# Kernel optimization log

Hardware: AMD Instinct MI355X
Metric: run time of the kernel (lower is better)

## Reference

```python
import jax, jax.numpy as jnp
import numpy as np

T0, T1, LENGTH = 844, 1264, 8137


def setup_inputs() -> dict:
    key = jax.random.key(0)
    kq, = jax.random.split(key, 1)
    q = jax.random.normal(kq, (4, 8, LENGTH), dtype=jnp.float32)
    alpha0 = jnp.array(0.4886, dtype=jnp.float32)
    alpha1 = jnp.array(0.3893, dtype=jnp.float32)
    return {"q": q, "alpha0": alpha0, "alpha1": alpha1}


def reference(q, alpha0, alpha1):
    # A = I + alpha0 * superdiag(offset T0) + alpha1 * superdiag(offset T1)
    A = (jnp.eye(LENGTH, dtype=q.dtype)
         + alpha0 * jnp.eye(LENGTH, k=T0, dtype=q.dtype)
         + alpha1 * jnp.eye(LENGTH, k=T1, dtype=q.dtype))
    A_inv = jnp.linalg.inv(A)          # [L, L] dense inverse
    x = q @ A_inv                       # [B, C, L]
    loss = jnp.sum(x[0, 0, -T1:] ** 2)  # scalar
    return loss
```

## Files before the change

### kernel.cpp

```cpp
#include <hip/hip_runtime.h>


#define LENGTH 8137
#define T0 844
#define T1 1264
#define JSTART (LENGTH - T1)
#define MMAX 9
#define NMAX 6

__global__ __launch_bounds__(256) void iir_loss_kernel(const float* __restrict__ q,
                                                       const float* __restrict__ a0p,
                                                       const float* __restrict__ a1p,
                                                       float* __restrict__ out) {
    __shared__ float xq[LENGTH];
    __shared__ float coef[NMAX + 1][MMAX + 1];
    __shared__ float partial[4];

    const int tid = threadIdx.x;
    const float a0 = a0p[0];
    const float a1 = a1p[0];

    const float4* q4 = reinterpret_cast<const float4*>(q);
    for (int i = tid; i < LENGTH / 4; i += 256) {
        float4 v = q4[i];
        xq[4 * i + 0] = v.x;
        xq[4 * i + 1] = v.y;
        xq[4 * i + 2] = v.z;
        xq[4 * i + 3] = v.w;
    }
    if (tid == 0) {
        xq[LENGTH - 1] = q[LENGTH - 1];
        coef[0][0] = 1.f;
        for (int m = 1; m <= MMAX; ++m) coef[0][m] = -a0 * coef[0][m - 1];
        for (int n = 1; n <= NMAX; ++n) {
            coef[n][0] = -a1 * coef[n - 1][0];
            for (int m = 1; m <= MMAX; ++m)
                coef[n][m] = -a0 * coef[n][m - 1] - a1 * coef[n - 1][m];
        }
    }
    __syncthreads();

    float v0 = 0.f, v1 = 0.f, v2 = 0.f, v3 = 0.f, v4 = 0.f;
    const int j0 = JSTART + tid;
    const bool has4 = (tid < (T1 - 4 * 256));

    for (int n = 0; n <= NMAX; ++n) {
        const int sn = T1 * n;
        for (int m = 0; m <= MMAX; ++m) {
            const int shift = sn + T0 * m;
            if (shift >= LENGTH) break;
            const float c = coef[n][m];
            const int off = j0 - shift;
            if (off >= 0)                 v0 += c * xq[off];
            if (off + 256 >= 0)           v1 += c * xq[off + 256];
            if (off + 512 >= 0)           v2 += c * xq[off + 512];
            if (off + 768 >= 0)           v3 += c * xq[off + 768];
            if (has4 && off + 1024 >= 0)  v4 += c * xq[off + 1024];
        }
    }

    float s = v0 * v0 + v1 * v1 + v2 * v2 + v3 * v3 + v4 * v4;

    for (int off = 32; off > 0; off >>= 1)
        s += __shfl_down(s, off, 64);
    if ((tid & 63) == 0) partial[tid >> 6] = s;
    __syncthreads();
    if (tid == 0)
        out[0] = partial[0] + partial[1] + partial[2] + partial[3];
}

extern "C" void kernel_launch(void* const* d_in, const int* in_sizes, int n_in,
                              void* d_out, int out_size, void* d_ws, size_t ws_size,
                              hipStream_t stream) {
    const float* q      = (const float*)d_in[0];
    const float* alpha0 = (const float*)d_in[1];
    const float* alpha1 = (const float*)d_in[2];
    float* out = (float*)d_out;

    iir_loss_kernel<<<1, 256, 0, stream>>>(q, alpha0, alpha1, out);
}
```

Baseline: 59.81 us.

## Use 1024 threads, per-thread register coefficients, and fully unrolled tap loop

Raises the single block from 256 to 1024 threads so each thread computes two outputs instead of five. The coefficient table is now computed redundantly in registers by every thread, which removes the serial single-thread setup phase and its shared-memory reads. The tap loops are fully unrolled so shifts are compile-time constants, and the final reduction grows to cover 16 wavefronts. The cost is more register pressure from the unrolled coefficient array, still on a single CU.

Result: no change. 59.59 us (-0.4%).

```diff
diff --git a/kernel.cpp b/kernel.cpp
--- a/kernel.cpp
+++ b/kernel.cpp
@@ -7,66 +7,72 @@
 #define JSTART (LENGTH - T1)
 #define MMAX 9
 #define NMAX 6
+#define NT 1024
 
-__global__ __launch_bounds__(256) void iir_loss_kernel(const float* __restrict__ q,
-                                                       const float* __restrict__ a0p,
-                                                       const float* __restrict__ a1p,
-                                                       float* __restrict__ out) {
+__global__ __launch_bounds__(1024) void iir_loss_kernel(const float* __restrict__ q,
+                                                        const float* __restrict__ a0p,
+                                                        const float* __restrict__ a1p,
+                                                        float* __restrict__ out) {
     __shared__ float xq[LENGTH];
-    __shared__ float coef[NMAX + 1][MMAX + 1];
-    __shared__ float partial[4];
+    __shared__ float partial[16];
 
     const int tid = threadIdx.x;
-    const float a0 = a0p[0];
-    const float a1 = a1p[0];
 
     const float4* q4 = reinterpret_cast<const float4*>(q);
-    for (int i = tid; i < LENGTH / 4; i += 256) {
+    for (int i = tid; i < LENGTH / 4; i += NT) {
         float4 v = q4[i];
         xq[4 * i + 0] = v.x;
         xq[4 * i + 1] = v.y;
         xq[4 * i + 2] = v.z;
         xq[4 * i + 3] = v.w;
     }
-    if (tid == 0) {
-        xq[LENGTH - 1] = q[LENGTH - 1];
-        coef[0][0] = 1.f;
-        for (int m = 1; m <= MMAX; ++m) coef[0][m] = -a0 * coef[0][m - 1];
-        for (int n = 1; n <= NMAX; ++n) {
-            coef[n][0] = -a1 * coef[n - 1][0];
-            for (int m = 1; m <= MMAX; ++m)
-                coef[n][m] = -a0 * coef[n][m - 1] - a1 * coef[n - 1][m];
-        }
+    if (tid == NT - 1) xq[LENGTH - 1] = q[LENGTH - 1];
+
+    const float a0 = a0p[0];
+    const float a1 = a1p[0];
+    float coef[NMAX + 1][MMAX + 1];
+    coef[0][0] = 1.f;
+#pragma unroll
+    for (int m = 1; m <= MMAX; ++m) coef[0][m] = -a0 * coef[0][m - 1];
+#pragma unroll
+    for (int n = 1; n <= NMAX; ++n) {
+        coef[n][0] = -a1 * coef[n - 1][0];
+#pragma unroll
+        for (int m = 1; m <= MMAX; ++m)
+            coef[n][m] = -a0 * coef[n][m - 1] - a1 * coef[n - 1][m];
     }
+
     __syncthreads();
 
-    float v0 = 0.f, v1 = 0.f, v2 = 0.f, v3 = 0.f, v4 = 0.f;
     const int j0 = JSTART + tid;
-    const bool has4 = (tid < (T1 - 4 * 256));
+    const bool has1 = (tid < (T1 - NT));
+    float v0 = 0.f, v1 = 0.f;
 
+#pragma unroll
     for (int n = 0; n <= NMAX; ++n) {
-        const int sn = T1 * n;
+#pragma unroll
         for (int m = 0; m <= MMAX; ++m) {
-            const int shift = sn + T0 * m;
-            if (shift >= LENGTH) break;
+            const int shift = T1 * n + T0 * m;
+            if (shift >= LENGTH) continue;
             const float c = coef[n][m];
             const int off = j0 - shift;
             if (off >= 0)                 v0 += c * xq[off];
-            if (off + 256 >= 0)           v1 += c * xq[off + 256];
-            if (off + 512 >= 0)           v2 += c * xq[off + 512];
-            if (off + 768 >= 0)           v3 += c * xq[off + 768];
-            if (has4 && off + 1024 >= 0)  v4 += c * xq[off + 1024];
+            if (has1 && off + NT >= 0)    v1 += c * xq[off + NT];
         }
     }
 
-    float s = v0 * v0 + v1 * v1 + v2 * v2 + v3 * v3 + v4 * v4;
+    float s = v0 * v0 + v1 * v1;
 
     for (int off = 32; off > 0; off >>= 1)
         s += __shfl_down(s, off, 64);
     if ((tid & 63) == 0) partial[tid >> 6] = s;
     __syncthreads();
-    if (tid == 0)
-        out[0] = partial[0] + partial[1] + partial[2] + partial[3];
+    if (tid < 64) {
+        float t = (tid < 16) ? partial[tid] : 0.f;
+        for (int off = 8; off > 0; off >>= 1)
+            t += __shfl_down(t, off, 64);
+        if (tid == 0) out[0] = t;
+    }
 }
 
 extern "C" void kernel_launch(void* const* d_in, const int* in_sizes, int n_in,
@@ -77,5 +83,5 @@
     const float* alpha1 = (const float*)d_in[2];
     float* out = (float*)d_out;
 
-    iir_loss_kernel<<<1, 256, 0, stream>>>(q, alpha0, alpha1, out);
+    iir_loss_kernel<<<1, NT, 0, stream>>>(q, alpha0, alpha1, out);
 }
```
